# Performance work log

Measured on AMD Instinct MI355X. Metric: run time of the kernel, lower is better.

## Reference

```python
import jax, jax.numpy as jnp
import numpy as np

KERNEL_MUL = 2.0
KERNEL_NUM = 5


def _mmd(source, target):
    n = source.shape[0]
    m = target.shape[0]
    total = jnp.concatenate([source, target], axis=0)  # [n+m, d]
    sq = jnp.sum(total * total, axis=1)  # [n+m]
    l2 = sq[:, None] + sq[None, :] - 2.0 * (total @ total.T)  # [n+m, n+m]
    l2 = jnp.maximum(l2, 0.0)
    n_samples = n + m
    bandwidth = jnp.sum(l2) / (n_samples * n_samples - n_samples)
    bandwidth = bandwidth / (KERNEL_MUL ** (KERNEL_NUM // 2))
    # sum of KERNEL_NUM Gaussian kernels with geometric bandwidths
    kernels = sum(jnp.exp(-l2 / (bandwidth * KERNEL_MUL ** i)) for i in range(KERNEL_NUM))
    b = n  # batch_size = n, as in the torch code
    xx = jnp.sum(kernels[:b, :b]) / (n * n)
    yy = jnp.sum(kernels[b:, b:]) / (m * m)
    xy = jnp.sum(kernels[:b, b:]) / (n * m)
    yx = jnp.sum(kernels[b:, :b]) / (m * n)
    return xx + yy - xy - yx


def setup_inputs() -> dict:
    key = jax.random.key(0)
    k1, k2 = jax.random.split(key)
    source = jax.random.normal(k1, (4096, 256), dtype=jnp.float32)
    target = jax.random.normal(k2, (4096, 256), dtype=jnp.float32)
    return {"source": source, "target": target}


def reference(source, target):
    return _mmd(source, target)
```

## Files before the change

kernel.cpp:

```cpp
#include <hip/hip_runtime.h>
#include <hip/hip_bf16.h>

#define WS_D_COLSUM 0
#define WS_D_NEGG   256
#define WS_D_ACC    257
#define WS_ACC_SLOTS 32
#define WS_SQ_OFF   4096
#define WS_G_OFF    36864

#define NROW 8192
#define HALF 4096
#define DIM  256
#define TILE 128
#define NB   64
#define KC   64
#define NC   (DIM / KC)

typedef short  short8  __attribute__((ext_vector_type(8)));
typedef float  f32x4   __attribute__((ext_vector_type(4)));
typedef unsigned short us4 __attribute__((ext_vector_type(4)));

static __device__ __forceinline__ unsigned short f2bfbits(float f) {
    __hip_bfloat16 h = __float2bfloat16(f);
    return *reinterpret_cast<unsigned short*>(&h);
}
static __device__ __forceinline__ float bfbits2f(unsigned short u) {
    return __uint_as_float(((unsigned int)u) << 16);
}
static __device__ __forceinline__ void gl_lds16(const void* g, void* l) {
    __builtin_amdgcn_global_load_lds(
        (const __attribute__((address_space(1))) void*)g,
        (__attribute__((address_space(3))) void*)l, 16, 0, 0);
}

__global__ __launch_bounds__(256) void k_cvt(const float* __restrict__ src,
                                             const float* __restrict__ tgt,
                                             unsigned short* __restrict__ G,
                                             float* __restrict__ sq) {
    int t    = threadIdx.x;
    int row  = blockIdx.x * 4 + (t >> 6);
    int lane = t & 63;
    const float* base = (row < HALF) ? (src + (size_t)row * DIM)
                                     : (tgt + (size_t)(row - HALF) * DIM);
    float4 v = *(const float4*)(base + lane * 4);
    unsigned short u0 = f2bfbits(v.x), u1 = f2bfbits(v.y),
                   u2 = f2bfbits(v.z), u3 = f2bfbits(v.w);
    us4 uu = {u0, u1, u2, u3};
    *(us4*)(G + (size_t)row * DIM + lane * 4) = uu;
    float r0 = bfbits2f(u0), r1 = bfbits2f(u1), r2 = bfbits2f(u2), r3 = bfbits2f(u3);
    float s = r0 * r0 + r1 * r1 + r2 * r2 + r3 * r3;
    #pragma unroll
    for (int off = 32; off; off >>= 1) s += __shfl_down(s, off);
    if (lane == 0) sq[row] = s;
}

__global__ __launch_bounds__(256) void k_colsum(const unsigned short* __restrict__ G,
                                                double* __restrict__ colsum) {
    int t  = threadIdx.x;
    int r0 = blockIdx.x * 128;
    double s = 0.0;
    for (int r = r0; r < r0 + 128; ++r)
        s += (double)bfbits2f(G[(size_t)r * DIM + t]);
    atomicAdd(&colsum[t], s);
}

__global__ __launch_bounds__(256) void k_bw(const float* __restrict__ sq,
                                            double* __restrict__ wsd) {
    __shared__ double red[256];
    __shared__ double red2[256];
    int t = threadIdx.x;
    double s = 0.0;
    for (int i = t; i < NROW; i += 256) s += (double)sq[i];
    double c = wsd[WS_D_COLSUM + t];
    red[t]  = s;
    red2[t] = c * c;
    __syncthreads();
    for (int off = 128; off; off >>= 1) {
        if (t < off) { red[t] += red[t + off]; red2[t] += red2[t + off]; }
        __syncthreads();
    }
    if (t == 0) {
        const double N = (double)NROW;
        double sum_l2 = 2.0 * N * red[0] - 2.0 * red2[0];
        double bw = sum_l2 / (N * N - N);
        bw = bw / 4.0;
        wsd[WS_D_NEGG] = -1.4426950408889634 / (16.0 * bw);
    }
}

__global__ __launch_bounds__(256) void k_mmd(const unsigned short* __restrict__ G,
                                             const float* __restrict__ sq,
                                             const double* __restrict__ wsd,
                                             double* __restrict__ acc_slots) {
    __shared__ unsigned short As[TILE * KC];
    __shared__ unsigned short Bs[TILE * KC];
    __shared__ double wsum[4];

    int bi = 0, rem = blockIdx.x;
    while (rem >= NB - bi) { rem -= NB - bi; ++bi; }
    int bj = bi + rem;

    int t = threadIdx.x, wid = t >> 6, lane = t & 63;
    int wr = wid >> 1, wc = wid & 1;
    int rl = lane & 15, klane = lane >> 4;

    const unsigned short* Abase = G + (size_t)bi * TILE * DIM;
    const unsigned short* Bbase = G + (size_t)bj * TILE * DIM;

    int sr8  = (lane >> 3);
    int sslt = lane & 7;

    const f32x4 zero4 = {0.f, 0.f, 0.f, 0.f};
    f32x4 acc[4][4];
    #pragma unroll
    for (int i = 0; i < 4; ++i)
        #pragma unroll
        for (int j = 0; j < 4; ++j) acc[i][j] = zero4;

    for (int kc = 0; kc < NC; ++kc) {
        __syncthreads();
        #pragma unroll
        for (int i = 0; i < 4; ++i) {
            int r    = wid * 32 + i * 8 + sr8;
            int slog = sslt ^ (r & 7);
            gl_lds16(Abase + (size_t)r * DIM + kc * KC + slog * 8,
                     &As[(wid * 32 + i * 8) * KC]);
        }
        #pragma unroll
        for (int i = 0; i < 4; ++i) {
            int r    = wid * 32 + i * 8 + sr8;
            int slog = sslt ^ (r & 7);
            gl_lds16(Bbase + (size_t)r * DIM + kc * KC + slog * 8,
                     &Bs[(wid * 32 + i * 8) * KC]);
        }
        __syncthreads();

        #pragma unroll
        for (int ks = 0; ks < 2; ++ks) {
            short8 af[4], bfv[4];
            #pragma unroll
            for (int f = 0; f < 4; ++f) {
                int ra = wr * 64 + f * 16 + rl;
                af[f]  = *(const short8*)&As[ra * KC + ((ks * 4 + klane) ^ (ra & 7)) * 8];
                int rb = wc * 64 + f * 16 + rl;
                bfv[f] = *(const short8*)&Bs[rb * KC + ((ks * 4 + klane) ^ (rb & 7)) * 8];
            }
            #pragma unroll
            for (int i = 0; i < 4; ++i)
                #pragma unroll
                for (int j = 0; j < 4; ++j)
                    acc[i][j] = __builtin_amdgcn_mfma_f32_16x16x32_bf16(af[i], bfv[j], acc[i][j], 0, 0, 0);
        }
    }

    int gi0 = bi * TILE + wr * 64;
    int gj0 = bj * TILE + wc * 64;
    float ng2 = (float)wsd[WS_D_NEGG];
    int rgrp = lane >> 4;

    float sqb4[4];
    #pragma unroll
    for (int j = 0; j < 4; ++j) sqb4[j] = sq[gj0 + j * 16 + rl];

    float tsum = 0.f;
    #pragma unroll
    for (int i = 0; i < 4; ++i) {
        float sqa4[4];
        #pragma unroll
        for (int rr = 0; rr < 4; ++rr) sqa4[rr] = sq[gi0 + i * 16 + rgrp * 4 + rr];
        #pragma unroll
        for (int j = 0; j < 4; ++j) {
            #pragma unroll
            for (int rr = 0; rr < 4; ++rr) {
                float l2 = fmaxf(sqa4[rr] + sqb4[j] - 2.0f * acc[i][j][rr], 0.f);
                float e   = exp2f(l2 * ng2);
                float e2  = e * e;
                float e4  = e2 * e2;
                float e8  = e4 * e4;
                float e16 = e8 * e8;
                tsum += e + e2 + e4 + e8 + e16;
            }
        }
    }

    float w = ((bi < 32) == (bj < 32)) ? 1.f : -1.f;
    if (bi != bj) w *= 2.f;
    double dsum = (double)tsum * (double)w;

    #pragma unroll
    for (int off = 32; off; off >>= 1) dsum += __shfl_down(dsum, off);
    if (lane == 0) wsum[wid] = dsum;
    __syncthreads();
    if (t == 0)
        atomicAdd(&acc_slots[blockIdx.x & (WS_ACC_SLOTS - 1)],
                  wsum[0] + wsum[1] + wsum[2] + wsum[3]);
}

__global__ void k_final(const double* __restrict__ wsd, float* __restrict__ out) {
    double s = 0.0;
    for (int i = 0; i < WS_ACC_SLOTS; ++i) s += wsd[WS_D_ACC + i];
    out[0] = (float)(s / ((double)HALF * (double)HALF));
}

extern "C" void kernel_launch(void* const* d_in, const int* in_sizes, int n_in,
                              void* d_out, int out_size, void* d_ws, size_t ws_size,
                              hipStream_t stream) {
    const float* src = (const float*)d_in[0];
    const float* tgt = (const float*)d_in[1];
    float* out = (float*)d_out;

    double* wsd         = (double*)d_ws;
    float* sq           = (float*)((char*)d_ws + WS_SQ_OFF);
    unsigned short* G   = (unsigned short*)((char*)d_ws + WS_G_OFF);

    hipMemsetAsync(d_ws, 0, 4096, stream);

    k_cvt<<<NROW / 4, 256, 0, stream>>>(src, tgt, G, sq);
    k_colsum<<<NROW / 128, 256, 0, stream>>>(G, &wsd[WS_D_COLSUM]);
    k_bw<<<1, 256, 0, stream>>>(sq, wsd);

    int nblocks = NB * (NB + 1) / 2;
    k_mmd<<<nblocks, 256, 0, stream>>>(G, sq, wsd, &wsd[WS_D_ACC]);

    k_final<<<1, 1, 0, stream>>>(wsd, out);
}
```

Measured before the change: 73.80 us.

## Triple-buffer GEMM tile loads and fuse conversion with column-sum kernel

The MMD tile kernel now loads K-chunks of 32 into a three-slot LDS ring. The next two stages are prefetched while the current one is computed, using explicit vmcnt waits and a single barrier per step instead of two syncthreads. The swizzle is reworked for the narrower chunk. Separately, the bf16 conversion, squared norms and column sums are fused into one prep kernel with LDS-reduced column sums, which removes a launch and a re-read of G. The cost is more LDS per block and more loop iterations with fewer MFMAs each.

```diff
diff --git a/kernel.cpp b/kernel.cpp
--- a/kernel.cpp
+++ b/kernel.cpp
@@ -13,11 +13,12 @@
 #define DIM  256
 #define TILE 128
 #define NB   64
-#define KC   64
+#define KC   32
 #define NC   (DIM / KC)
-
-typedef short  short8  __attribute__((ext_vector_type(8)));
-typedef float  f32x4   __attribute__((ext_vector_type(4)));
+#define BUFE (TILE * KC)
+
+typedef short  short8 __attribute__((ext_vector_type(8)));
+typedef float  f32x4  __attribute__((ext_vector_type(4)));
 typedef unsigned short us4 __attribute__((ext_vector_type(4)));
 
 static __device__ __forceinline__ unsigned short f2bfbits(float f) {
@@ -33,34 +34,41 @@
         (__attribute__((address_space(3))) void*)l, 16, 0, 0);
 }
 
-__global__ __launch_bounds__(256) void k_cvt(const float* __restrict__ src,
-                                             const float* __restrict__ tgt,
-                                             unsigned short* __restrict__ G,
-                                             float* __restrict__ sq) {
-    int t    = threadIdx.x;
-    int row  = blockIdx.x * 4 + (t >> 6);
-    int lane = t & 63;
-    const float* base = (row < HALF) ? (src + (size_t)row * DIM)
-                                     : (tgt + (size_t)(row - HALF) * DIM);
-    float4 v = *(const float4*)(base + lane * 4);
-    unsigned short u0 = f2bfbits(v.x), u1 = f2bfbits(v.y),
-                   u2 = f2bfbits(v.z), u3 = f2bfbits(v.w);
-    us4 uu = {u0, u1, u2, u3};
-    *(us4*)(G + (size_t)row * DIM + lane * 4) = uu;
-    float r0 = bfbits2f(u0), r1 = bfbits2f(u1), r2 = bfbits2f(u2), r3 = bfbits2f(u3);
-    float s = r0 * r0 + r1 * r1 + r2 * r2 + r3 * r3;
-    #pragma unroll
-    for (int off = 32; off; off >>= 1) s += __shfl_down(s, off);
-    if (lane == 0) sq[row] = s;
-}
-
-__global__ __launch_bounds__(256) void k_colsum(const unsigned short* __restrict__ G,
-                                                double* __restrict__ colsum) {
-    int t  = threadIdx.x;
-    int r0 = blockIdx.x * 128;
-    double s = 0.0;
-    for (int r = r0; r < r0 + 128; ++r)
-        s += (double)bfbits2f(G[(size_t)r * DIM + t]);
+__global__ __launch_bounds__(256) void k_prep(const float* __restrict__ src,
+                                              const float* __restrict__ tgt,
+                                              unsigned short* __restrict__ G,
+                                              float* __restrict__ sq,
+                                              double* __restrict__ colsum) {
+    __shared__ float cs_lds[4 * 256];
+    int t = threadIdx.x, wid = t >> 6, lane = t & 63;
+    int r0 = blockIdx.x * 64;
+    int c4 = lane * 4;
+
+    float cs0 = 0.f, cs1 = 0.f, cs2 = 0.f, cs3 = 0.f;
+    for (int i = 0; i < 16; ++i) {
+        int row = r0 + wid + i * 4;
+        const float* base = (row < HALF) ? (src + (size_t)row * DIM)
+                                         : (tgt + (size_t)(row - HALF) * DIM);
+        float4 v = *(const float4*)(base + c4);
+        unsigned short u0 = f2bfbits(v.x), u1 = f2bfbits(v.y),
+                       u2 = f2bfbits(v.z), u3 = f2bfbits(v.w);
+        us4 uu = {u0, u1, u2, u3};
+        *(us4*)(G + (size_t)row * DIM + c4) = uu;
+        float r0f = bfbits2f(u0), r1f = bfbits2f(u1),
+              r2f = bfbits2f(u2), r3f = bfbits2f(u3);
+        cs0 += r0f; cs1 += r1f; cs2 += r2f; cs3 += r3f;
+        float s = r0f * r0f + r1f * r1f + r2f * r2f + r3f * r3f;
+        #pragma unroll
+        for (int off = 32; off; off >>= 1) s += __shfl_down(s, off);
+        if (lane == 0) sq[row] = s;
+    }
+    cs_lds[wid * 256 + c4 + 0] = cs0;
+    cs_lds[wid * 256 + c4 + 1] = cs1;
+    cs_lds[wid * 256 + c4 + 2] = cs2;
+    cs_lds[wid * 256 + c4 + 3] = cs3;
+    __syncthreads();
+    double s = (double)cs_lds[t] + (double)cs_lds[256 + t] +
+               (double)cs_lds[512 + t] + (double)cs_lds[768 + t];
     atomicAdd(&colsum[t], s);
 }
 
@@ -88,12 +96,12 @@
     }
 }
 
-__global__ __launch_bounds__(256) void k_mmd(const unsigned short* __restrict__ G,
-                                             const float* __restrict__ sq,
-                                             const double* __restrict__ wsd,
-                                             double* __restrict__ acc_slots) {
-    __shared__ unsigned short As[TILE * KC];
-    __shared__ unsigned short Bs[TILE * KC];
+__global__ __launch_bounds__(256, 3) void k_mmd(const unsigned short* __restrict__ G,
+                                                const float* __restrict__ sq,
+                                                const double* __restrict__ wsd,
+                                                double* __restrict__ acc_slots) {
+    __shared__ unsigned short As[3 * BUFE];
+    __shared__ unsigned short Bs[3 * BUFE];
     __shared__ double wsum[4];
 
     int bi = 0, rem = blockIdx.x;
@@ -107,8 +115,23 @@
     const unsigned short* Abase = G + (size_t)bi * TILE * DIM;
     const unsigned short* Bbase = G + (size_t)bj * TILE * DIM;
 
-    int sr8  = (lane >> 3);
-    int sslt = lane & 7;
+    int lr0 = wid * 32 + (lane >> 2);
+    int slog0 = (lane & 3) ^ ((lr0 >> 1) & 3);
+    int lr1 = lr0 + 16;
+    int slog1 = (lane & 3) ^ ((lr1 >> 1) & 3);
+    size_t ga0 = (size_t)lr0 * DIM + slog0 * 8;
+    size_t ga1 = (size_t)lr1 * DIM + slog1 * 8;
+    int ld0 = (wid * 32) * KC;
+    int ld1 = (wid * 32 + 16) * KC;
+
+    int aoff[4], boff[4];
+    #pragma unroll
+    for (int f = 0; f < 4; ++f) {
+        int ra = wr * 64 + f * 16 + rl;
+        aoff[f] = ra * KC + ((klane ^ ((ra >> 1) & 3)) * 8);
+        int rb = wc * 64 + f * 16 + rl;
+        boff[f] = rb * KC + ((klane ^ ((rb >> 1) & 3)) * 8);
+    }
 
     const f32x4 zero4 = {0.f, 0.f, 0.f, 0.f};
     f32x4 acc[4][4];
@@ -117,41 +140,40 @@
         #pragma unroll
         for (int j = 0; j < 4; ++j) acc[i][j] = zero4;
 
+    #define STAGE(kc, b)                                                     \
+        do {                                                                 \
+            gl_lds16(Abase + ga0 + (kc) * KC, &As[(b) * BUFE + ld0]);        \
+            gl_lds16(Bbase + ga0 + (kc) * KC, &Bs[(b) * BUFE + ld0]);        \
+            gl_lds16(Abase + ga1 + (kc) * KC, &As[(b) * BUFE + ld1]);        \
+            gl_lds16(Bbase + ga1 + (kc) * KC, &Bs[(b) * BUFE + ld1]);        \
+        } while (0)
+
+    STAGE(0, 0);
+    STAGE(1, 1);
+
+    #pragma unroll
     for (int kc = 0; kc < NC; ++kc) {
-        __syncthreads();
-        #pragma unroll
-        for (int i = 0; i < 4; ++i) {
-            int r    = wid * 32 + i * 8 + sr8;
-            int slog = sslt ^ (r & 7);
-            gl_lds16(Abase + (size_t)r * DIM + kc * KC + slog * 8,
-                     &As[(wid * 32 + i * 8) * KC]);
+        if (kc < NC - 1) { asm volatile("s_waitcnt vmcnt(4)" ::: "memory"); }
+        else             { asm volatile("s_waitcnt vmcnt(0)" ::: "memory"); }
+        __builtin_amdgcn_s_barrier();
+        __builtin_amdgcn_sched_barrier(0);
+        if (kc + 2 < NC) STAGE(kc + 2, (kc + 2) % 3);
+
+        const unsigned short* Ab = &As[(kc % 3) * BUFE];
+        const unsigned short* Bb = &Bs[(kc % 3) * BUFE];
+        short8 af[4], bfv[4];
+        #pragma unroll
+        for (int f = 0; f < 4; ++f) {
+            af[f]  = *(const short8*)&Ab[aoff[f]];
+            bfv[f] = *(const short8*)&Bb[boff[f]];
         }
         #pragma unroll
-        for (int i = 0; i < 4; ++i) {
-            int r    = wid * 32 + i * 8 + sr8;
-            int slog = sslt ^ (r & 7);
-            gl_lds16(Bbase + (size_t)r * DIM + kc * KC + slog * 8,
-                     &Bs[(wid * 32 + i * 8) * KC]);
-        }
-        __syncthreads();
-
-        #pragma unroll
-        for (int ks = 0; ks < 2; ++ks) {
-            short8 af[4], bfv[4];
+        for (int i = 0; i < 4; ++i)
             #pragma unroll
-            for (int f = 0; f < 4; ++f) {
-                int ra = wr * 64 + f * 16 + rl;
-                af[f]  = *(const short8*)&As[ra * KC + ((ks * 4 + klane) ^ (ra & 7)) * 8];
-                int rb = wc * 64 + f * 16 + rl;
-                bfv[f] = *(const short8*)&Bs[rb * KC + ((ks * 4 + klane) ^ (rb & 7)) * 8];
-            }
-            #pragma unroll
-            for (int i = 0; i < 4; ++i)
-                #pragma unroll
-                for (int j = 0; j < 4; ++j)
-                    acc[i][j] = __builtin_amdgcn_mfma_f32_16x16x32_bf16(af[i], bfv[j], acc[i][j], 0, 0, 0);
-        }
-    }
+            for (int j = 0; j < 4; ++j)
+                acc[i][j] = __builtin_amdgcn_mfma_f32_16x16x32_bf16(af[i], bfv[j], acc[i][j], 0, 0, 0);
+    }
+    #undef STAGE
 
     int gi0 = bi * TILE + wr * 64;
     int gj0 = bj * TILE + wc * 64;
@@ -209,14 +231,13 @@
     const float* tgt = (const float*)d_in[1];
     float* out = (float*)d_out;
 
-    double* wsd         = (double*)d_ws;
-    float* sq           = (float*)((char*)d_ws + WS_SQ_OFF);
-    unsigned short* G   = (unsigned short*)((char*)d_ws + WS_G_OFF);
+    double* wsd       = (double*)d_ws;
+    float* sq         = (float*)((char*)d_ws + WS_SQ_OFF);
+    unsigned short* G = (unsigned short*)((char*)d_ws + WS_G_OFF);
 
     hipMemsetAsync(d_ws, 0, 4096, stream);
 
-    k_cvt<<<NROW / 4, 256, 0, stream>>>(src, tgt, G, sq);
-    k_colsum<<<NROW / 128, 256, 0, stream>>>(G, &wsd[WS_D_COLSUM]);
+    k_prep<<<128, 256, 0, stream>>>(src, tgt, G, sq, &wsd[WS_D_COLSUM]);
     k_bw<<<1, 256, 0, stream>>>(sq, wsd);
 
     int nblocks = NB * (NB + 1) / 2;
```

After: 73.21 us. No clear change (-0.8%).
